# Kernel optimization log

Hardware: AMD Instinct MI355X
Metric: run time of the kernel (lower is better)

The kernel has to match this reference:

```python
import jax, jax.numpy as jnp
import numpy as np

D_MODEL, N_HEADS = 1024, 16
D_H = D_MODEL // N_HEADS          # 64
D_HR = D_H // 2                   # 32 (decoupled RoPE dim)
D_LATENT = 256
THETA = 10000.0


def rope(x, theta=THETA):
    # x: (..., S, d) with d even; rotate interleaved pairs.
    S, d = x.shape[-2], x.shape[-1]
    inv = theta ** (-jnp.arange(0, d, 2, dtype=jnp.float32) / d)      # (d/2,)
    ang = jnp.arange(S, dtype=jnp.float32)[:, None] * inv             # (S, d/2)
    cos, sin = jnp.cos(ang), jnp.sin(ang)
    x1, x2 = x[..., 0::2], x[..., 1::2]
    r1 = x1 * cos - x2 * sin
    r2 = x1 * sin + x2 * cos
    return jnp.stack([r1, r2], axis=-1).reshape(x.shape)


def setup_inputs() -> dict:
    key = jax.random.key(0)
    ks = jax.random.split(key, 9)
    s = lambda fan_in: 1.0 / np.sqrt(fan_in)
    return {
        "x": jax.random.normal(ks[0], (4, 2048, D_MODEL), jnp.float32),
        "W_DQ": jax.random.normal(ks[1], (D_MODEL, D_LATENT), jnp.float32) * s(D_MODEL),
        "W_UQ": jax.random.normal(ks[2], (D_LATENT, N_HEADS * D_H), jnp.float32) * s(D_LATENT),
        "W_QR": jax.random.normal(ks[3], (D_LATENT, N_HEADS * D_HR), jnp.float32) * s(D_LATENT),
        "W_DKV": jax.random.normal(ks[4], (D_MODEL, D_LATENT), jnp.float32) * s(D_MODEL),
        "W_UK": jax.random.normal(ks[5], (D_LATENT, N_HEADS * D_H), jnp.float32) * s(D_LATENT),
        "W_UV": jax.random.normal(ks[6], (D_LATENT, N_HEADS * D_H), jnp.float32) * s(D_LATENT),
        "W_KR": jax.random.normal(ks[7], (D_MODEL, D_HR), jnp.float32) * s(D_MODEL),
        "W_O": jax.random.normal(ks[8], (N_HEADS * D_H, D_MODEL), jnp.float32) * s(N_HEADS * D_H),
    }


def reference(x, W_DQ, W_UQ, W_QR, W_DKV, W_UK, W_UV, W_KR, W_O):
    B, S, _ = x.shape
    d_qk = D_H + D_HR

    # --- query path: low-rank latent + decoupled RoPE ---
    c_q = x @ W_DQ                                                   # (B,S,L)
    Qc = (c_q @ W_UQ).reshape(B, S, N_HEADS, D_H).transpose(0, 2, 1, 3)   # (B,H,S,dh)
    Qr = (c_q @ W_QR).reshape(B, S, N_HEADS, D_HR).transpose(0, 2, 1, 3)  # (B,H,S,dhr)
    Qr = rope(Qr)

    # --- key/value path: shared latent, shared rotary key ---
    c_kv = x @ W_DKV                                                 # (B,S,L)
    Kc = (c_kv @ W_UK).reshape(B, S, N_HEADS, D_H).transpose(0, 2, 1, 3)  # (B,H,S,dh)
    Kr = rope((x @ W_KR)[:, None, :, :])                             # (B,1,S,dhr)
    Kr = jnp.broadcast_to(Kr, (B, N_HEADS, S, D_HR))
    V = (c_kv @ W_UV).reshape(B, S, N_HEADS, D_H).transpose(0, 2, 1, 3)   # (B,H,S,dh)

    Q = jnp.concatenate([Qc, Qr], axis=-1)                           # (B,H,S,d_qk)
    K = jnp.concatenate([Kc, Kr], axis=-1)

    scores = jnp.einsum('bhqd,bhkd->bhqk', Q, K)
    scores = jnp.clip(scores, -80.0, 80.0)
    causal = jnp.tril(jnp.ones((S, S), dtype=bool))
    scores = jnp.where(causal, scores, -jnp.inf)
    weights = jax.nn.softmax(scores / jnp.sqrt(jnp.float32(d_qk)), axis=-1)
    attn = jnp.einsum('bhqk,bhkd->bhqd', weights, V)                 # (B,H,S,dh)
    attn = attn.transpose(0, 2, 1, 3).reshape(B, S, N_HEADS * D_H)
    return attn @ W_O
```

## Files before the change

### kernel.cpp

```cpp
#include <hip/hip_runtime.h>
#include <hip/hip_bf16.h>


typedef __attribute__((ext_vector_type(8))) __bf16 bf16x8;
typedef __attribute__((ext_vector_type(4))) float f32x4;
typedef __attribute__((ext_vector_type(16))) float f32x16;
typedef __attribute__((ext_vector_type(4))) unsigned short us4;

#define DEV static __device__ __forceinline__

DEV unsigned short f2b(float f) {
  union { __hip_bfloat16 h; unsigned short u; } v;
  v.h = __float2bfloat16(f);
  return v.u;
}
DEV float b2f(unsigned short u) {
  union { unsigned short u; __hip_bfloat16 h; } v;
  v.u = u;
  return __bfloat162float(v.h);
}
DEV unsigned int f2b2(float lo, float hi) {
  union { __hip_bfloat162 h2; unsigned int u; } v;
  float2 t; t.x = lo; t.y = hi;
  v.h2 = __float22bfloat162_rn(t);
  return v.u;
}
DEV f32x4 mfma16(bf16x8 a, bf16x8 b, f32x4 c) {
  return __builtin_amdgcn_mfma_f32_16x16x32_bf16(a, b, c, 0, 0, 0);
}
DEV f32x16 mfma32(bf16x8 a, bf16x8 b, f32x16 c) {
  return __builtin_amdgcn_mfma_f32_32x32x16_bf16(a, b, c, 0, 0, 0);
}
DEV void load_lds16(const void* g, void* lds) {
  __builtin_amdgcn_global_load_lds((__attribute__((address_space(1))) void*)g,
                                   (__attribute__((address_space(3))) void*)lds,
                                   16, 0, 0);
}

#define KSC2f 0.14724444690f
#define CLIPf 11.7795557220f

struct TWArgs { const float* W[8]; unsigned short* T[8]; };
__global__ __launch_bounds__(256) void prep(const float* __restrict__ x,
                                            unsigned short* __restrict__ xb, TWArgs a) {
  if (blockIdx.x < 8192) {
    long i = (long)(blockIdx.x * 256 + threadIdx.x) * 4;
    float4 v = *(const float4*)(x + i);
    us4 o = { f2b(v.x), f2b(v.y), f2b(v.z), f2b(v.w) };
    *(us4*)(xb + i) = o;
    return;
  }
  int bid = blockIdx.x - 8192;
  int g;
  if      (bid < 256)  g = 0;
  else if (bid < 512)  g = 1;
  else if (bid < 544)  g = 2;
  else if (bid < 800)  g = 3;
  else if (bid < 928)  g = 4;
  else if (bid < 1184) g = 5;
  else if (bid < 1440) g = 6;
  else                 g = 7;
  const int starts[8] = {0, 256, 512, 544, 800, 928, 1184, 1440};
  int local = bid - starts[g];
  int K = (g >= 3 && g <= 6) ? 256 : 1024;
  int N = (g < 2) ? 256 : (g == 2 ? 32 : (g == 4 ? 512 : 1024));
  int tilesX = N >> 5;
  int n0 = (local % tilesX) * 32, k0 = (local / tilesX) * 32;
  const float* W = a.W[g];
  unsigned short* WT = a.T[g];
  float sc = (g == 3 || g == 4) ? KSC2f : 1.0f;
  __shared__ float tile[32][33];
  int tx = threadIdx.x & 31, ty = threadIdx.x >> 5;
#pragma unroll
  for (int i = 0; i < 32; i += 8)
    tile[ty + i][tx] = W[(size_t)(k0 + ty + i) * N + n0 + tx];
  __syncthreads();
#pragma unroll
  for (int i = 0; i < 32; i += 8)
    WT[(size_t)(n0 + ty + i) * K + k0 + tx] = f2b(tile[tx][ty + i] * sc);
}

__global__ __launch_bounds__(256) void rope_qk(unsigned short* __restrict__ C2,
                                               const unsigned short* __restrict__ C1,
                                               unsigned short* __restrict__ Krr) {
  if (blockIdx.x < 8192) {
    int idx = blockIdx.x * 256 + threadIdx.x;
    int i = idx & 15, h = (idx >> 4) & 15, s = (idx >> 8) & 2047, b = idx >> 19;
    long base = (long)(b * 2048 + s) * 1536 + 1024 + h * 32 + 2 * i;
    float x1 = b2f(C2[base]), x2 = b2f(C2[base + 1]);
    float inv = exp2f(-(float)i * 0.8304820237686285f);
    float ang = (float)s * inv;
    float c = cosf(ang), sn = sinf(ang);
    C2[base]     = f2b(x1 * c - x2 * sn);
    C2[base + 1] = f2b(x1 * sn + x2 * c);
  } else {
    int idx = (blockIdx.x - 8192) * 256 + threadIdx.x;
    int i = idx & 15, s = (idx >> 4) & 2047, b = idx >> 15;
    long src = (long)(b * 2048 + s) * 544 + 512 + 2 * i;
    float x1 = b2f(C1[src]), x2 = b2f(C1[src + 1]);
    float inv = exp2f(-(float)i * 0.8304820237686285f);
    float ang = (float)s * inv;
    float c = cosf(ang), sn = sinf(ang);
    long dst = (long)(b * 2048 + s) * 32 + 2 * i;
    Krr[dst]     = f2b(x1 * c - x2 * sn);
    Krr[dst + 1] = f2b(x1 * sn + x2 * c);
  }
}

template <bool OUT_BF16>
__global__ __launch_bounds__(256) void gemm_bt(const unsigned short* __restrict__ A, int lda,
                                               const unsigned short* __restrict__ Bt, int ldb,
                                               void* __restrict__ Cv, int ldc, int N, int K) {
  __shared__ __align__(16) unsigned short As[128 * 32];
  __shared__ __align__(16) unsigned short Bs[128 * 32];
  const int t = threadIdx.x;
  const int w = t >> 6, lane = t & 63, ln = lane & 15, quad = lane >> 4;
  const int wr = w >> 1, wc = w & 1;
  const int bm0 = blockIdx.x * 128, bn0 = blockIdx.y * 128;
  const int srow = t >> 2;
  const int scol = (t & 3) * 8;
  f32x4 zero = {0.f, 0.f, 0.f, 0.f};
  f32x4 acc[4][4];
#pragma unroll
  for (int i = 0; i < 4; ++i)
#pragma unroll
    for (int j = 0; j < 4; ++j) acc[i][j] = zero;

  for (int k0 = 0; k0 < K; k0 += 32) {
#pragma unroll
    for (int r = 0; r < 2; ++r) {
      int arow = bm0 + r * 64 + srow;
      load_lds16(A + (long)arow * lda + k0 + scol, (char*)As + r * 4096 + w * 1024);
      int brow = bn0 + r * 64 + srow;
      if (brow > N - 1) brow = N - 1;
      load_lds16(Bt + (long)brow * ldb + k0 + scol, (char*)Bs + r * 4096 + w * 1024);
    }
    __syncthreads();
    bf16x8 af[4], bf[4];
#pragma unroll
    for (int i = 0; i < 4; ++i)
      af[i] = *(const bf16x8*)(As + (wr * 64 + i * 16 + ln) * 32 + quad * 8);
#pragma unroll
    for (int j = 0; j < 4; ++j)
      bf[j] = *(const bf16x8*)(Bs + (wc * 64 + j * 16 + ln) * 32 + quad * 8);
#pragma unroll
    for (int i = 0; i < 4; ++i)
#pragma unroll
      for (int j = 0; j < 4; ++j) acc[i][j] = mfma16(af[i], bf[j], acc[i][j]);
    __syncthreads();
  }
#pragma unroll
  for (int i = 0; i < 4; ++i)
#pragma unroll
    for (int j = 0; j < 4; ++j)
#pragma unroll
      for (int r = 0; r < 4; ++r) {
        int row = bm0 + wr * 64 + i * 16 + quad * 4 + r;
        int col = bn0 + wc * 64 + j * 16 + ln;
        if (col < N) {
          if (OUT_BF16)
            ((unsigned short*)Cv)[(long)row * ldc + col] = f2b(acc[i][j][r]);
          else
            ((float*)Cv)[(long)row * ldc + col] = acc[i][j][r];
        }
      }
}

__global__ __launch_bounds__(256) void gemm_kv(const unsigned short* __restrict__ A, int lda,
                                               const unsigned short* __restrict__ Bt0,
                                               unsigned short* __restrict__ C3,
                                               unsigned short* __restrict__ Vt) {
  __shared__ __align__(16) unsigned short As[128 * 32];
  __shared__ __align__(16) unsigned short Bs[128 * 32];
  const int t = threadIdx.x;
  const int w = t >> 6, lane = t & 63, ln = lane & 15, quad = lane >> 4;
  const int wr = w >> 1, wc = w & 1;
  const bool isV = blockIdx.y >= 8;
  const unsigned short* Bt = Bt0 + (isV ? (size_t)1024 * 256 : 0);
  const int bm0 = blockIdx.x * 128, bn0 = (blockIdx.y & 7) * 128;
  const int srow = t >> 2, scol = (t & 3) * 8;
  f32x4 zero = {0.f, 0.f, 0.f, 0.f};
  f32x4 acc[4][4];
#pragma unroll
  for (int i = 0; i < 4; ++i)
#pragma unroll
    for (int j = 0; j < 4; ++j) acc[i][j] = zero;

  for (int k0 = 0; k0 < 256; k0 += 32) {
#pragma unroll
    for (int r = 0; r < 2; ++r) {
      load_lds16(A + (long)(bm0 + r * 64 + srow) * lda + k0 + scol, (char*)As + r * 4096 + w * 1024);
      load_lds16(Bt + (long)(bn0 + r * 64 + srow) * 256 + k0 + scol, (char*)Bs + r * 4096 + w * 1024);
    }
    __syncthreads();
    bf16x8 af[4], bf[4];
#pragma unroll
    for (int i = 0; i < 4; ++i)
      af[i] = *(const bf16x8*)(As + (wr * 64 + i * 16 + ln) * 32 + quad * 8);
#pragma unroll
    for (int j = 0; j < 4; ++j)
      bf[j] = *(const bf16x8*)(Bs + (wc * 64 + j * 16 + ln) * 32 + quad * 8);
#pragma unroll
    for (int i = 0; i < 4; ++i)
#pragma unroll
      for (int j = 0; j < 4; ++j) acc[i][j] = mfma16(af[i], bf[j], acc[i][j]);
    __syncthreads();
  }
  if (!isV) {
#pragma unroll
    for (int i = 0; i < 4; ++i)
#pragma unroll
      for (int j = 0; j < 4; ++j)
#pragma unroll
        for (int r = 0; r < 4; ++r) {
          int row = bm0 + wr * 64 + i * 16 + quad * 4 + r;
          int col = bn0 + wc * 64 + j * 16 + ln;
          C3[(long)row * 1024 + col] = f2b(acc[i][j][r]);
        }
  } else {
#pragma unroll
    for (int i = 0; i < 4; ++i)
#pragma unroll
      for (int j = 0; j < 4; ++j) {
        int col = bn0 + wc * 64 + j * 16 + ln;
        int row0 = bm0 + wr * 64 + i * 16 + quad * 4;
        int b = row0 >> 11, sl = row0 & 2047;
        us4 pk = { f2b(acc[i][j][0]), f2b(acc[i][j][1]), f2b(acc[i][j][2]), f2b(acc[i][j][3]) };
        *(us4*)(Vt + ((size_t)(b * 16) * 64 + col) * 2048 + sl) = pk;
      }
  }
}

__global__ __launch_bounds__(256, 3) void flash_attn(const unsigned short* __restrict__ C2,
                                                     const unsigned short* __restrict__ C3,
                                                     const unsigned short* __restrict__ Krr,
                                                     const unsigned short* __restrict__ Vt,
                                                     unsigned short* __restrict__ Oa) {
  __shared__ __align__(16) unsigned short Ks[2][4096];
  __shared__ __align__(16) unsigned short Vs[2][4096];

  const int tid = threadIdx.x;
  const int w = tid >> 6, lane = tid & 63;
  const int l31 = lane & 31, h = lane >> 5;
  const int bh = blockIdx.x, b = bh >> 4, head = bh & 15;
  const int bS = b * 2048;
  const int qi = 15 - (int)blockIdx.y;
  const int qb = qi * 128 + w * 32;
  const int nkt = 2 * qi + 2;
  const int q = qb + l31;
  const int pr = (l31 & ~12) | ((l31 & 4) << 1) | ((l31 & 8) >> 1);

  const unsigned short* qp = C2 + (size_t)(bS + q) * 1536;
  bf16x8 qf[6];
#pragma unroll
  for (int c = 0; c < 4; ++c)
    qf[c] = *(const bf16x8*)(qp + head * 64 + c * 16 + h * 8);
#pragma unroll
  for (int c = 4; c < 6; ++c)
    qf[c] = *(const bf16x8*)(qp + 1024 + head * 32 + (c - 4) * 16 + h * 8);

  union { unsigned short u[8]; bf16x8 v; } onesu;
#pragma unroll
  for (int i = 0; i < 8; ++i) onesu.u[i] = 0x3F80;
  const bf16x8 ones = onesu.v;

  f32x16 o0 = {}, o1 = {}, osum = {};

  auto stage = [&](int buf, int key0) {
#pragma unroll
    for (int t = w; t < 8; t += 4) {
      int ci = t * 64 + lane;
      int r = ci >> 3, sl = ci & 7;
      int srcc = sl ^ (r & 7) ^ (r >> 3);
      int srck = (r & ~12) | ((r & 4) << 1) | ((r & 8) >> 1);
      load_lds16(C3 + (size_t)(bS + key0 + srck) * 1024 + head * 64 + srcc * 8,
                 &Ks[buf][t * 512]);
    }
#pragma unroll
    for (int t = w; t < 8; t += 4) {
      int ci = t * 64 + lane;
      int r = ci >> 3, sl = ci & 7;
      int srcc = sl ^ (r & 7) ^ (r >> 3);
      load_lds16(Vt + (size_t)((size_t)bh * 64 + r) * 2048 + key0 + srcc * 8,
                 &Vs[buf][t * 512]);
    }
  };

  stage(0, 0);
  for (int kt = 0; kt < nkt; ++kt) {
    __syncthreads();
    const int c0 = kt * 64;
    const bool live = (c0 <= qb + 31);
    bf16x8 kr[4];
    if (live) {
#pragma unroll
      for (int m = 0; m < 2; ++m)
#pragma unroll
        for (int c = 0; c < 2; ++c)
          kr[m * 2 + c] = *(const bf16x8*)(Krr + (size_t)(bS + c0 + m * 32 + pr) * 32 +
                                           c * 16 + h * 8);
    }
    if (kt + 1 < nkt) stage((kt + 1) & 1, c0 + 64);
    if (!live) continue;

    const unsigned short* Kp = Ks[kt & 1];
    const unsigned short* Vp = Vs[kt & 1];

#pragma unroll
    for (int m = 0; m < 2; ++m) {
      if (c0 + m * 32 > qb + 31) continue;
      const int r = m * 32 + l31;
      f32x16 s = {};
#pragma unroll
      for (int c = 0; c < 4; ++c) {
        int slot = (2 * c + h) ^ (r & 7) ^ (r >> 3);
        bf16x8 kf = *(const bf16x8*)(Kp + r * 64 + slot * 8);
        s = mfma32(kf, qf[c], s);
      }
      s = mfma32(kr[m * 2 + 0], qf[4], s);
      s = mfma32(kr[m * 2 + 1], qf[5], s);

      const bool nm = (c0 + m * 32 + 31) > qb;
      float ev[16];
#pragma unroll
      for (int p = 0; p < 16; ++p) {
        float z = __builtin_amdgcn_fmed3f(s[p], -CLIPf, CLIPf);
        if (nm) {
          int key = c0 + m * 32 + (p & 3) + 4 * ((p >> 2) & 1) + 8 * h + 16 * (p >> 3);
          if (key > q) z = -1e30f;
        }
        ev[p] = exp2f(z);
      }
      bf16x8 pf[2];
#pragma unroll
      for (int t = 0; t < 2; ++t) {
        union { unsigned int u[4]; bf16x8 v; } pk;
#pragma unroll
        for (int j = 0; j < 4; ++j)
          pk.u[j] = f2b2(ev[t * 8 + 2 * j], ev[t * 8 + 2 * j + 1]);
        pf[t] = pk.v;
      }
#pragma unroll
      for (int t = 0; t < 2; ++t) {
        int tk = m * 2 + t;
        osum = mfma32(pf[t], ones, osum);
#pragma unroll
        for (int n = 0; n < 2; ++n) {
          int rr = n * 32 + l31;
          int slot = (2 * tk + h) ^ (rr & 7) ^ (rr >> 3);
          bf16x8 vf = *(const bf16x8*)(Vp + rr * 64 + slot * 8);
          if (n == 0) o0 = mfma32(pf[t], vf, o0);
          else        o1 = mfma32(pf[t], vf, o1);
        }
      }
    }
  }

#pragma unroll
  for (int p = 0; p < 16; ++p) {
    int qrow = (p & 3) + 8 * (p >> 2) + 4 * h;
    float rl = 1.0f / osum[p];
    size_t base = (size_t)(bS + qb + qrow) * 1024 + head * 64;
    Oa[base + l31]      = f2b(o0[p] * rl);
    Oa[base + 32 + l31] = f2b(o1[p] * rl);
  }
}

extern "C" void kernel_launch(void* const* d_in, const int* in_sizes, int n_in,
                              void* d_out, int out_size, void* d_ws, size_t ws_size,
                              hipStream_t stream) {
  (void)in_sizes; (void)n_in; (void)out_size; (void)ws_size;
  const float* x     = (const float*)d_in[0];
  const float* W_DQ  = (const float*)d_in[1];
  const float* W_UQ  = (const float*)d_in[2];
  const float* W_QR  = (const float*)d_in[3];
  const float* W_DKV = (const float*)d_in[4];
  const float* W_UK  = (const float*)d_in[5];
  const float* W_UV  = (const float*)d_in[6];
  const float* W_KR  = (const float*)d_in[7];
  const float* W_O   = (const float*)d_in[8];

  char* p = (char*)d_ws;
  unsigned short* xb  = (unsigned short*)p; p += (size_t)8192 * 1024 * 2;
  unsigned short* WT1 = (unsigned short*)p; p += (size_t)544 * 1024 * 2;
  unsigned short* WT2 = (unsigned short*)p; p += (size_t)1536 * 256 * 2;
  unsigned short* WT3 = (unsigned short*)p; p += (size_t)2048 * 256 * 2;
  unsigned short* WT4 = (unsigned short*)p; p += (size_t)1024 * 1024 * 2;
  unsigned short* C1  = (unsigned short*)p; p += (size_t)8192 * 544 * 2;
  unsigned short* C2  = (unsigned short*)p; p += (size_t)8192 * 1536 * 2;
  unsigned short* C3  = (unsigned short*)p; p += (size_t)8192 * 1024 * 2;
  unsigned short* Krr = (unsigned short*)p; p += (size_t)8192 * 32 * 2;
  unsigned short* Vt  = (unsigned short*)p; p += (size_t)64 * 64 * 2048 * 2;
  unsigned short* Oa  = (unsigned short*)p; p += (size_t)8192 * 1024 * 2;

  TWArgs tw;
  tw.W[0] = W_DQ;  tw.T[0] = WT1;
  tw.W[1] = W_DKV; tw.T[1] = WT1 + 256 * 1024;
  tw.W[2] = W_KR;  tw.T[2] = WT1 + 512 * 1024;
  tw.W[3] = W_UQ;  tw.T[3] = WT2;
  tw.W[4] = W_QR;  tw.T[4] = WT2 + 1024 * 256;
  tw.W[5] = W_UK;  tw.T[5] = WT3;
  tw.W[6] = W_UV;  tw.T[6] = WT3 + 1024 * 256;
  tw.W[7] = W_O;   tw.T[7] = WT4;
  prep<<<8192 + 2464, 256, 0, stream>>>(x, xb, tw);

  gemm_bt<true><<<dim3(64, 5),  256, 0, stream>>>(xb, 1024, WT1, 1024, C1, 544, 544, 1024);
  gemm_bt<true><<<dim3(64, 12), 256, 0, stream>>>(C1, 544, WT2, 256, C2, 1536, 1536, 256);
  gemm_kv<<<dim3(64, 16),       256, 0, stream>>>(C1 + 256, 544, WT3, C3, Vt);
  rope_qk<<<8704, 256, 0, stream>>>(C2, C1, Krr);
  flash_attn<<<dim3(64, 16), 256, 0, stream>>>(C2, C3, Krr, Vt, Oa);
  gemm_bt<false><<<dim3(64, 8), 256, 0, stream>>>(Oa, 1024, WT4, 1024, d_out, 1024, 1024, 1024);
}
```

Before: 276.8 us.

## Fuse RoPE into GEMM epilogues and merge Q/K/V up-projections into one launch

Removes the standalone rope_qk kernel by applying the rotary rotation in the GEMM epilogues: the key rotary part in the down-projection GEMM and the query rotary part in the up-projection GEMM, with pair swaps done via lane shuffles. It also merges the Q up-projection GEMM and the K/V up-projection GEMM into one 28-column-block launch. This saves a read-modify-write pass over the rotary columns and two kernel launches, and gives the merged GEMM more blocks to run concurrently. The cost is extra sin/cos work and shuffles in some epilogues, plus more branching in the fused kernel.

```diff
diff --git a/kernel.cpp b/kernel.cpp
--- a/kernel.cpp
+++ b/kernel.cpp
@@ -13,11 +13,6 @@
   union { __hip_bfloat16 h; unsigned short u; } v;
   v.h = __float2bfloat16(f);
   return v.u;
-}
-DEV float b2f(unsigned short u) {
-  union { unsigned short u; __hip_bfloat16 h; } v;
-  v.u = u;
-  return __bfloat162float(v.h);
 }
 DEV unsigned int f2b2(float lo, float hi) {
   union { __hip_bfloat162 h2; unsigned int u; } v;
@@ -39,6 +34,7 @@
 
 #define KSC2f 0.14724444690f
 #define CLIPf 11.7795557220f
+#define RINVf 0.8304820237686285f
 
 struct TWArgs { const float* W[8]; unsigned short* T[8]; };
 __global__ __launch_bounds__(256) void prep(const float* __restrict__ x,
@@ -80,30 +76,169 @@
     WT[(size_t)(n0 + ty + i) * K + k0 + tx] = f2b(tile[tx][ty + i] * sc);
 }
 
-__global__ __launch_bounds__(256) void rope_qk(unsigned short* __restrict__ C2,
-                                               const unsigned short* __restrict__ C1,
+__global__ __launch_bounds__(256) void gemm_dq(const unsigned short* __restrict__ A,
+                                               const unsigned short* __restrict__ Bt,
+                                               unsigned short* __restrict__ C1,
                                                unsigned short* __restrict__ Krr) {
-  if (blockIdx.x < 8192) {
-    int idx = blockIdx.x * 256 + threadIdx.x;
-    int i = idx & 15, h = (idx >> 4) & 15, s = (idx >> 8) & 2047, b = idx >> 19;
-    long base = (long)(b * 2048 + s) * 1536 + 1024 + h * 32 + 2 * i;
-    float x1 = b2f(C2[base]), x2 = b2f(C2[base + 1]);
-    float inv = exp2f(-(float)i * 0.8304820237686285f);
-    float ang = (float)s * inv;
-    float c = cosf(ang), sn = sinf(ang);
-    C2[base]     = f2b(x1 * c - x2 * sn);
-    C2[base + 1] = f2b(x1 * sn + x2 * c);
+  __shared__ __align__(16) unsigned short As[128 * 32];
+  __shared__ __align__(16) unsigned short Bs[128 * 32];
+  const int t = threadIdx.x;
+  const int w = t >> 6, lane = t & 63, ln = lane & 15, quad = lane >> 4;
+  const int wr = w >> 1, wc = w & 1;
+  const int bm0 = blockIdx.x * 128, bn0 = blockIdx.y * 128;
+  const int srow = t >> 2, scol = (t & 3) * 8;
+  f32x4 zero = {0.f, 0.f, 0.f, 0.f};
+  f32x4 acc[4][4];
+#pragma unroll
+  for (int i = 0; i < 4; ++i)
+#pragma unroll
+    for (int j = 0; j < 4; ++j) acc[i][j] = zero;
+
+  for (int k0 = 0; k0 < 1024; k0 += 32) {
+#pragma unroll
+    for (int r = 0; r < 2; ++r) {
+      load_lds16(A + (long)(bm0 + r * 64 + srow) * 1024 + k0 + scol, (char*)As + r * 4096 + w * 1024);
+      int brow = bn0 + r * 64 + srow;
+      if (brow > 543) brow = 543;
+      load_lds16(Bt + (long)brow * 1024 + k0 + scol, (char*)Bs + r * 4096 + w * 1024);
+    }
+    __syncthreads();
+    bf16x8 af[4], bf[4];
+#pragma unroll
+    for (int i = 0; i < 4; ++i)
+      af[i] = *(const bf16x8*)(As + (wr * 64 + i * 16 + ln) * 32 + quad * 8);
+#pragma unroll
+    for (int j = 0; j < 4; ++j)
+      bf[j] = *(const bf16x8*)(Bs + (wc * 64 + j * 16 + ln) * 32 + quad * 8);
+#pragma unroll
+    for (int i = 0; i < 4; ++i)
+#pragma unroll
+      for (int j = 0; j < 4; ++j) acc[i][j] = mfma16(af[i], bf[j], acc[i][j]);
+    __syncthreads();
+  }
+  const bool kr = (blockIdx.y == 4) && (wc == 0);
+#pragma unroll
+  for (int i = 0; i < 4; ++i)
+#pragma unroll
+    for (int j = 0; j < 4; ++j)
+#pragma unroll
+      for (int r = 0; r < 4; ++r) {
+        int row = bm0 + wr * 64 + i * 16 + quad * 4 + r;
+        int col = bn0 + wc * 64 + j * 16 + ln;
+        float v = acc[i][j][r];
+        if (kr && j < 2) {
+          float pv = __shfl_xor(v, 1);
+          int kc = j * 16 + ln;
+          float inv = exp2f(-(float)(kc >> 1) * RINVf);
+          float ang = (float)(row & 2047) * inv;
+          float c = cosf(ang), sn = sinf(ang);
+          float out = (ln & 1) ? fmaf(pv, sn, v * c) : fmaf(v, c, -(pv * sn));
+          Krr[(size_t)row * 32 + kc] = f2b(out);
+        }
+        if (col < 544)
+          C1[(long)row * 544 + col] = f2b(v);
+      }
+}
+
+__global__ __launch_bounds__(256) void gemm_mid(const unsigned short* __restrict__ C1,
+                                                const unsigned short* __restrict__ WT2,
+                                                const unsigned short* __restrict__ WT3,
+                                                unsigned short* __restrict__ C2,
+                                                unsigned short* __restrict__ C3,
+                                                unsigned short* __restrict__ Vt) {
+  __shared__ __align__(16) unsigned short As[128 * 32];
+  __shared__ __align__(16) unsigned short Bs[128 * 32];
+  const int t = threadIdx.x;
+  const int w = t >> 6, lane = t & 63, ln = lane & 15, quad = lane >> 4;
+  const int wr = w >> 1, wc = w & 1;
+  const int y = blockIdx.y;
+  const unsigned short* A;
+  const unsigned short* Bt;
+  int bn0;
+  if (y < 12)      { A = C1;       Bt = WT2;                       bn0 = y * 128; }
+  else if (y < 20) { A = C1 + 256; Bt = WT3;                       bn0 = (y - 12) * 128; }
+  else             { A = C1 + 256; Bt = WT3 + (size_t)1024 * 256;  bn0 = (y - 20) * 128; }
+  const int bm0 = blockIdx.x * 128;
+  const int srow = t >> 2, scol = (t & 3) * 8;
+  f32x4 zero = {0.f, 0.f, 0.f, 0.f};
+  f32x4 acc[4][4];
+#pragma unroll
+  for (int i = 0; i < 4; ++i)
+#pragma unroll
+    for (int j = 0; j < 4; ++j) acc[i][j] = zero;
+
+  for (int k0 = 0; k0 < 256; k0 += 32) {
+#pragma unroll
+    for (int r = 0; r < 2; ++r) {
+      load_lds16(A + (long)(bm0 + r * 64 + srow) * 544 + k0 + scol, (char*)As + r * 4096 + w * 1024);
+      load_lds16(Bt + (long)(bn0 + r * 64 + srow) * 256 + k0 + scol, (char*)Bs + r * 4096 + w * 1024);
+    }
+    __syncthreads();
+    bf16x8 af[4], bf[4];
+#pragma unroll
+    for (int i = 0; i < 4; ++i)
+      af[i] = *(const bf16x8*)(As + (wr * 64 + i * 16 + ln) * 32 + quad * 8);
+#pragma unroll
+    for (int j = 0; j < 4; ++j)
+      bf[j] = *(const bf16x8*)(Bs + (wc * 64 + j * 16 + ln) * 32 + quad * 8);
+#pragma unroll
+    for (int i = 0; i < 4; ++i)
+#pragma unroll
+      for (int j = 0; j < 4; ++j) acc[i][j] = mfma16(af[i], bf[j], acc[i][j]);
+    __syncthreads();
+  }
+
+  if (y < 8) {
+#pragma unroll
+    for (int i = 0; i < 4; ++i)
+#pragma unroll
+      for (int j = 0; j < 4; ++j)
+#pragma unroll
+        for (int r = 0; r < 4; ++r) {
+          int row = bm0 + wr * 64 + i * 16 + quad * 4 + r;
+          int col = bn0 + wc * 64 + j * 16 + ln;
+          C2[(long)row * 1536 + col] = f2b(acc[i][j][r]);
+        }
+  } else if (y < 12) {
+#pragma unroll
+    for (int i = 0; i < 4; ++i)
+#pragma unroll
+      for (int j = 0; j < 4; ++j)
+#pragma unroll
+        for (int r = 0; r < 4; ++r) {
+          int row = bm0 + wr * 64 + i * 16 + quad * 4 + r;
+          int col = bn0 + wc * 64 + j * 16 + ln;
+          float v = acc[i][j][r];
+          float pv = __shfl_xor(v, 1);
+          int hc = ((j & 1) << 4) | ln;
+          float inv = exp2f(-(float)(hc >> 1) * RINVf);
+          float ang = (float)(row & 2047) * inv;
+          float c = cosf(ang), sn = sinf(ang);
+          float out = (ln & 1) ? fmaf(pv, sn, v * c) : fmaf(v, c, -(pv * sn));
+          C2[(long)row * 1536 + col] = f2b(out);
+        }
+  } else if (y < 20) {
+#pragma unroll
+    for (int i = 0; i < 4; ++i)
+#pragma unroll
+      for (int j = 0; j < 4; ++j)
+#pragma unroll
+        for (int r = 0; r < 4; ++r) {
+          int row = bm0 + wr * 64 + i * 16 + quad * 4 + r;
+          int col = bn0 + wc * 64 + j * 16 + ln;
+          C3[(long)row * 1024 + col] = f2b(acc[i][j][r]);
+        }
   } else {
-    int idx = (blockIdx.x - 8192) * 256 + threadIdx.x;
-    int i = idx & 15, s = (idx >> 4) & 2047, b = idx >> 15;
-    long src = (long)(b * 2048 + s) * 544 + 512 + 2 * i;
-    float x1 = b2f(C1[src]), x2 = b2f(C1[src + 1]);
-    float inv = exp2f(-(float)i * 0.8304820237686285f);
-    float ang = (float)s * inv;
-    float c = cosf(ang), sn = sinf(ang);
-    long dst = (long)(b * 2048 + s) * 32 + 2 * i;
-    Krr[dst]     = f2b(x1 * c - x2 * sn);
-    Krr[dst + 1] = f2b(x1 * sn + x2 * c);
+#pragma unroll
+    for (int i = 0; i < 4; ++i)
+#pragma unroll
+      for (int j = 0; j < 4; ++j) {
+        int col = bn0 + wc * 64 + j * 16 + ln;
+        int row0 = bm0 + wr * 64 + i * 16 + quad * 4;
+        int b = row0 >> 11, sl = row0 & 2047;
+        us4 pk = { f2b(acc[i][j][0]), f2b(acc[i][j][1]), f2b(acc[i][j][2]), f2b(acc[i][j][3]) };
+        *(us4*)(Vt + ((size_t)(b * 16) * 64 + col) * 2048 + sl) = pk;
+      }
   }
 }
 
@@ -117,8 +252,7 @@
   const int w = t >> 6, lane = t & 63, ln = lane & 15, quad = lane >> 4;
   const int wr = w >> 1, wc = w & 1;
   const int bm0 = blockIdx.x * 128, bn0 = blockIdx.y * 128;
-  const int srow = t >> 2;
-  const int scol = (t & 3) * 8;
+  const int srow = t >> 2, scol = (t & 3) * 8;
   f32x4 zero = {0.f, 0.f, 0.f, 0.f};
   f32x4 acc[4][4];
 #pragma unroll
@@ -129,8 +263,7 @@
   for (int k0 = 0; k0 < K; k0 += 32) {
 #pragma unroll
     for (int r = 0; r < 2; ++r) {
-      int arow = bm0 + r * 64 + srow;
-      load_lds16(A + (long)arow * lda + k0 + scol, (char*)As + r * 4096 + w * 1024);
+      load_lds16(A + (long)(bm0 + r * 64 + srow) * lda + k0 + scol, (char*)As + r * 4096 + w * 1024);
       int brow = bn0 + r * 64 + srow;
       if (brow > N - 1) brow = N - 1;
       load_lds16(Bt + (long)brow * ldb + k0 + scol, (char*)Bs + r * 4096 + w * 1024);
@@ -164,71 +297,6 @@
             ((float*)Cv)[(long)row * ldc + col] = acc[i][j][r];
         }
       }
-}
-
-__global__ __launch_bounds__(256) void gemm_kv(const unsigned short* __restrict__ A, int lda,
-                                               const unsigned short* __restrict__ Bt0,
-                                               unsigned short* __restrict__ C3,
-                                               unsigned short* __restrict__ Vt) {
-  __shared__ __align__(16) unsigned short As[128 * 32];
-  __shared__ __align__(16) unsigned short Bs[128 * 32];
-  const int t = threadIdx.x;
-  const int w = t >> 6, lane = t & 63, ln = lane & 15, quad = lane >> 4;
-  const int wr = w >> 1, wc = w & 1;
-  const bool isV = blockIdx.y >= 8;
-  const unsigned short* Bt = Bt0 + (isV ? (size_t)1024 * 256 : 0);
-  const int bm0 = blockIdx.x * 128, bn0 = (blockIdx.y & 7) * 128;
-  const int srow = t >> 2, scol = (t & 3) * 8;
-  f32x4 zero = {0.f, 0.f, 0.f, 0.f};
-  f32x4 acc[4][4];
-#pragma unroll
-  for (int i = 0; i < 4; ++i)
-#pragma unroll
-    for (int j = 0; j < 4; ++j) acc[i][j] = zero;
-
-  for (int k0 = 0; k0 < 256; k0 += 32) {
-#pragma unroll
-    for (int r = 0; r < 2; ++r) {
-      load_lds16(A + (long)(bm0 + r * 64 + srow) * lda + k0 + scol, (char*)As + r * 4096 + w * 1024);
-      load_lds16(Bt + (long)(bn0 + r * 64 + srow) * 256 + k0 + scol, (char*)Bs + r * 4096 + w * 1024);
-    }
-    __syncthreads();
-    bf16x8 af[4], bf[4];
-#pragma unroll
-    for (int i = 0; i < 4; ++i)
-      af[i] = *(const bf16x8*)(As + (wr * 64 + i * 16 + ln) * 32 + quad * 8);
-#pragma unroll
-    for (int j = 0; j < 4; ++j)
-      bf[j] = *(const bf16x8*)(Bs + (wc * 64 + j * 16 + ln) * 32 + quad * 8);
-#pragma unroll
-    for (int i = 0; i < 4; ++i)
-#pragma unroll
-      for (int j = 0; j < 4; ++j) acc[i][j] = mfma16(af[i], bf[j], acc[i][j]);
-    __syncthreads();
-  }
-  if (!isV) {
-#pragma unroll
-    for (int i = 0; i < 4; ++i)
-#pragma unroll
-      for (int j = 0; j < 4; ++j)
-#pragma unroll
-        for (int r = 0; r < 4; ++r) {
-          int row = bm0 + wr * 64 + i * 16 + quad * 4 + r;
-          int col = bn0 + wc * 64 + j * 16 + ln;
-          C3[(long)row * 1024 + col] = f2b(acc[i][j][r]);
-        }
-  } else {
-#pragma unroll
-    for (int i = 0; i < 4; ++i)
-#pragma unroll
-      for (int j = 0; j < 4; ++j) {
-        int col = bn0 + wc * 64 + j * 16 + ln;
-        int row0 = bm0 + wr * 64 + i * 16 + quad * 4;
-        int b = row0 >> 11, sl = row0 & 2047;
-        us4 pk = { f2b(acc[i][j][0]), f2b(acc[i][j][1]), f2b(acc[i][j][2]), f2b(acc[i][j][3]) };
-        *(us4*)(Vt + ((size_t)(b * 16) * 64 + col) * 2048 + sl) = pk;
-      }
-  }
 }
 
 __global__ __launch_bounds__(256, 3) void flash_attn(const unsigned short* __restrict__ C2,
@@ -404,10 +472,8 @@
   tw.W[7] = W_O;   tw.T[7] = WT4;
   prep<<<8192 + 2464, 256, 0, stream>>>(x, xb, tw);
 
-  gemm_bt<true><<<dim3(64, 5),  256, 0, stream>>>(xb, 1024, WT1, 1024, C1, 544, 544, 1024);
-  gemm_bt<true><<<dim3(64, 12), 256, 0, stream>>>(C1, 544, WT2, 256, C2, 1536, 1536, 256);
-  gemm_kv<<<dim3(64, 16),       256, 0, stream>>>(C1 + 256, 544, WT3, C3, Vt);
-  rope_qk<<<8704, 256, 0, stream>>>(C2, C1, Krr);
+  gemm_dq<<<dim3(64, 5),   256, 0, stream>>>(xb, WT1, C1, Krr);
+  gemm_mid<<<dim3(64, 28), 256, 0, stream>>>(C1, WT2, WT3, C2, C3, Vt);
   flash_attn<<<dim3(64, 16), 256, 0, stream>>>(C2, C3, Krr, Vt, Oa);
   gemm_bt<false><<<dim3(64, 8), 256, 0, stream>>>(Oa, 1024, WT4, 1024, d_out, 1024, 1024, 1024);
 }
```

New measurement: 517.8 us. +87.0%, slower.
